# Kernel tuning notes

Hardware: AMD Instinct MI355X
Metric: run time of the kernel (lower is better)

The kernel has to match this reference:

```python
import jax, jax.numpy as jnp
import numpy as np

N = 20000      # num_nodes / scatter_size
F = 128        # dataset_num_features
H = 8          # heads
HID = 64       # hidden_channels
REP = 512      # represent_features
NCLS = 133     # dataset_num_classes
E = 200000     # num edges (== num synapses)
PTS = 4        # points per synapse
P = E * PTS    # total synapse points

# Eval-mode semantics: dropout = identity; PyG MLP BatchNorm with fresh
# running stats (mean=0, var=1, affine=1/0) = identity. GATConv has no
# edge_dim, so edge_attr does not enter the math (kept as an input for parity).

def _glorot(key, shape):
    fan_in, fan_out = shape[0], shape[-1]
    if len(shape) == 3:  # attention vectors [H, C]: PyG treats as (1, H*C)
        fan_in, fan_out = 1, shape[-2] * shape[-1]
    lim = jnp.sqrt(6.0 / (fan_in + fan_out))
    return jax.random.uniform(key, shape, jnp.float32, -lim, lim)


def setup_inputs() -> dict:
    key = jax.random.key(0)
    ks = jax.random.split(key, 20)
    edge_index = jax.random.randint(ks[0], (2, E), 0, N, dtype=jnp.int32)
    edge_attr = jax.random.normal(ks[1], (E, 1), jnp.float32)
    synapse = jax.random.normal(ks[2], (P, 6), jnp.float32)
    # every synapse (edge) owns PTS points -> no empty segments for max-pool
    synapse_index = (jnp.arange(P, dtype=jnp.int32) // PTS)
    inp = {
        "edge_index": edge_index,
        "edge_attr": edge_attr,
        "synapse": synapse,
        "synapse_index": synapse_index,
        "scatter_size": N,
        # learned node embedding (nn.Parameter, xavier)
        "x_param": _glorot(ks[3], (N, F)),
        # GATConv 1: F -> H*HID
        "W1": _glorot(ks[4], (F, H * HID)),
        "att_src1": _glorot(ks[5], (1, H, HID))[0],
        "att_dst1": _glorot(ks[6], (1, H, HID))[0],
        "b1": jnp.zeros((H * HID,), jnp.float32),
        # GATConv 2: H*HID -> REP, heads=1, concat=False
        "W2": _glorot(ks[7], (H * HID, REP)),
        "att_src2": _glorot(ks[8], (1, 1, REP))[0],
        "att_dst2": _glorot(ks[9], (1, 1, REP))[0],
        "b2": jnp.zeros((REP,), jnp.float32),
        # synapse_encoder MLP([6, 256, 512])
        "We1": _glorot(ks[10], (6, 256)),
        "be1": jnp.zeros((256,), jnp.float32),
        "We2": _glorot(ks[11], (256, 512)),
        "be2": jnp.zeros((512,), jnp.float32),
        # classmodel MLP([1536, 512, 133])
        "Wc1": _glorot(ks[12], (1536, 512)),
        "bc1": jnp.zeros((512,), jnp.float32),
        "Wc2": _glorot(ks[13], (512, NCLS)),
        "bc2": jnp.zeros((NCLS,), jnp.float32),
    }
    return inp


def _gat_conv(x, src, dst, n, W, a_src, a_dst, b, heads, ch, concat):
    # x: [n, Fin]; src/dst already include self-loops (PyG default)
    xl = (x @ W).reshape(n, heads, ch)                 # [n, H, C]
    s = jnp.einsum('nhc,hc->nh', xl, a_src)            # alpha_src
    d = jnp.einsum('nhc,hc->nh', xl, a_dst)            # alpha_dst
    alpha = jax.nn.leaky_relu(s[src] + d[dst], negative_slope=0.2)  # [Ee, H]
    amax = jax.ops.segment_max(alpha, dst, num_segments=n)
    ex = jnp.exp(alpha - amax[dst])
    den = jax.ops.segment_sum(ex, dst, num_segments=n)
    a = ex / (den[dst] + 1e-16)                        # segment softmax
    out = jax.ops.segment_sum(xl[src] * a[:, :, None], dst, num_segments=n)
    out = out.reshape(n, heads * ch) if concat else out.mean(axis=1)
    return out + b


def _scatter_mean(vals, idx, n):
    s = jax.ops.segment_sum(vals, idx, num_segments=n)
    cnt = jax.ops.segment_sum(jnp.ones((vals.shape[0],), vals.dtype), idx, num_segments=n)
    return s / jnp.maximum(cnt, 1.0)[:, None]


def reference(edge_index, edge_attr, synapse, synapse_index, scatter_size,
              x_param, W1, att_src1, att_dst1, b1, W2, att_src2, att_dst2, b2,
              We1, be1, We2, be2, Wc1, bc1, Wc2, bc2):
    n = scatter_size
    loop = jnp.arange(n, dtype=edge_index.dtype)
    src = jnp.concatenate([edge_index[0], loop])   # GATConv adds self-loops
    dst = jnp.concatenate([edge_index[1], loop])

    x = jax.nn.elu(_gat_conv(x_param, src, dst, n, W1, att_src1, att_dst1, b1, H, HID, True))
    x = _gat_conv(x, src, dst, n, W2, att_src2, att_dst2, b2, 1, REP, False)   # [n, REP]

    # global_max_pool over synapse points -> one 6-vec per edge
    x_point = jax.ops.segment_max(synapse, synapse_index, num_segments=E)      # [E, 6]
    x_point = jax.nn.relu(x_point @ We1 + be1) @ We2 + be2                      # [E, 512]

    left = _scatter_mean(x_point, edge_index[0], n)
    right = _scatter_mean(x_point, edge_index[1], n)

    final = jnp.concatenate([x, left, right], axis=1)                           # [n, 1536]
    pred = jax.nn.relu(final @ Wc1 + bc1) @ Wc2 + bc2
    return pred
```

## Files before the change

kernel.cpp:

```cpp
#include <hip/hip_runtime.h>
#include <cstddef>

#define NN   20000
#define FEAT 128
#define NH   8
#define NE   200000
#define EE   220000

typedef _Float16 f16;
typedef _Float16 f16x2 __attribute__((ext_vector_type(2)));
typedef _Float16 f16x4 __attribute__((ext_vector_type(4)));
typedef _Float16 f16x8 __attribute__((ext_vector_type(8)));
typedef float    f32x4 __attribute__((ext_vector_type(4)));

__device__ __forceinline__ float lrelu(float a) { return a > 0.f ? a : 0.2f * a; }
__device__ __forceinline__ float rdlane(float v, int l) {
  return __int_as_float(__builtin_amdgcn_readlane(__float_as_int(v), l));
}
__device__ __forceinline__ void gld_lds16(const f16* g, f16* l) {
  __builtin_amdgcn_global_load_lds(
      (const __attribute__((address_space(1))) void*)g,
      (__attribute__((address_space(3))) void*)l, 16, 0, 0);
}

#define QB0 128
#define QB1 (QB0 + 8)
#define QB2 (QB1 + 80)
#define QB3 (QB2 + 64)
#define QB4 (QB3 + 782)
#define QB5 (QB4 + 1250)
__global__ __launch_bounds__(256) void preamble(
    const int* __restrict__ ei, const float* __restrict__ syn,
    const float* __restrict__ W1, const float* __restrict__ xparam,
    const float* __restrict__ W2, const float* __restrict__ We2,
    const float* __restrict__ Wc1, const float* __restrict__ Wc2,
    const float* __restrict__ b2, const float* __restrict__ be2,
    const float* __restrict__ as2, const float* __restrict__ ad2,
    int* __restrict__ dL, int* __restrict__ dR,
    float* __restrict__ xp, f16* __restrict__ W1t, f16* __restrict__ xph,
    f16* __restrict__ WzAt, f16* __restrict__ McatT, f16* __restrict__ Wc2t,
    float* __restrict__ vB, float* __restrict__ vL, float* __restrict__ vR,
    float* __restrict__ ws2, float* __restrict__ wd2)
{
  __shared__ float smem[2112];
  const int b = blockIdx.x, t = threadIdx.x;
  if (b < QB0) {
    float (*As)[68] = (float(*)[68])smem;
    float (*Bs)[64] = (float(*)[64])(smem + 16 * 68);
    const int bb = b;
    const float* A; const float* B; f16* dst; int dstOff, m0, n0;
    if (bb < 64)      { A = W2;  B = Wc1;  dst = WzAt;  dstOff = 0;
                        m0 = (bb >> 3) * 64; n0 = (bb & 7) * 64; }
    else if (bb < 96) { int i = bb - 64; A = We2; B = Wc1 + (size_t)512 * 512;
                        dst = McatT; dstOff = 0;
                        m0 = (i >> 3) * 64; n0 = (i & 7) * 64; }
    else              { int i = bb - 96; A = We2; B = Wc1 + (size_t)1024 * 512;
                        dst = McatT; dstOff = 256;
                        m0 = (i >> 3) * 64; n0 = (i & 7) * 64; }
    const int tx = t & 15, ty = t >> 4;
    float acc[4][4] = {{0.f}};
    float pa[4], pb[4];
#pragma unroll
    for (int i = 0; i < 4; i++) {
      int idx = t + i * 256;
      pa[i] = A[(size_t)(m0 + (idx >> 4)) * 512 + (idx & 15)];
      pb[i] = B[(size_t)(idx >> 6) * 512 + n0 + (idx & 63)];
    }
    for (int k0 = 0; k0 < 512; k0 += 16) {
#pragma unroll
      for (int i = 0; i < 4; i++) {
        int idx = t + i * 256;
        As[idx & 15][idx >> 4] = pa[i];
        Bs[idx >> 6][idx & 63] = pb[i];
      }
      __syncthreads();
      if (k0 + 16 < 512) {
        int kn = k0 + 16;
#pragma unroll
        for (int i = 0; i < 4; i++) {
          int idx = t + i * 256;
          pa[i] = A[(size_t)(m0 + (idx >> 4)) * 512 + kn + (idx & 15)];
          pb[i] = B[(size_t)(kn + (idx >> 6)) * 512 + n0 + (idx & 63)];
        }
      }
#pragma unroll
      for (int kk = 0; kk < 16; kk++) {
        float4 a4 = *(const float4*)&As[kk][ty * 4];
        float4 b4 = *(const float4*)&Bs[kk][tx * 4];
        float av[4] = {a4.x, a4.y, a4.z, a4.w};
        float bv[4] = {b4.x, b4.y, b4.z, b4.w};
#pragma unroll
        for (int i = 0; i < 4; i++)
#pragma unroll
          for (int j = 0; j < 4; j++) acc[i][j] = fmaf(av[i], bv[j], acc[i][j]);
      }
      __syncthreads();
    }
#pragma unroll
    for (int i = 0; i < 4; i++)
#pragma unroll
      for (int j = 0; j < 4; j++)
        dst[(size_t)(n0 + tx * 4 + j) * 512 + dstOff + m0 + ty * 4 + i] = (f16)acc[i][j];
  } else if (b < QB1) {
    int g = (b - QB0) * 256 + t;
    int seg = g >> 9, j = g & 511;
    if (seg == 0) {
      float a = 0.f;
      for (int k = 0; k < 512; k++) a = fmaf(b2[k], Wc1[(size_t)k * 512 + j], a);
      vB[j] = a;
    } else if (seg == 1) {
      float a = 0.f;
      for (int k = 0; k < 512; k++) a = fmaf(be2[k], Wc1[(size_t)(512 + k) * 512 + j], a);
      vL[j] = a;
    } else if (seg == 2) {
      float a = 0.f;
      for (int k = 0; k < 512; k++) a = fmaf(be2[k], Wc1[(size_t)(1024 + k) * 512 + j], a);
      vR[j] = a;
    } else {
      float a = 0.f, c2 = 0.f;
      for (int c = 0; c < 512; c++) {
        float w = W2[(size_t)j * 512 + c];
        a = fmaf(w, as2[c], a);
        c2 = fmaf(w, ad2[c], c2);
      }
      ws2[j] = a; wd2[j] = c2;
    }
  } else if (b < QB2) {
    float (*tile)[33] = (float(*)[33])smem;
    int i0 = b - QB1;
    const int n0 = (i0 % 5) * 32, k0 = (i0 / 5) * 32;
    const int tx = t & 31, ty = t >> 5;
#pragma unroll
    for (int i = 0; i < 4; i++) {
      int k = k0 + ty + i * 8, n = n0 + tx;
      tile[ty + i * 8][tx] = (n < 133) ? Wc2[(size_t)k * 133 + n] : 0.f;
    }
    __syncthreads();
#pragma unroll
    for (int i = 0; i < 4; i++) {
      int n = n0 + ty + i * 8, k = k0 + tx;
      if (n < 133) Wc2t[(size_t)n * 512 + k] = (f16)tile[tx][ty + i * 8];
    }
  } else if (b < QB3) {
    float (*tile)[33] = (float(*)[33])smem;
    int bb = b - QB2;
    const int n0 = (bb & 15) * 32, k0 = (bb >> 4) * 32;
    const int tx = t & 31, ty = t >> 5;
#pragma unroll
    for (int i = 0; i < 4; i++)
      tile[ty + i * 8][tx] = W1[(size_t)(k0 + ty + i * 8) * 512 + n0 + tx];
    __syncthreads();
#pragma unroll
    for (int i = 0; i < 4; i++)
      W1t[(size_t)(n0 + ty + i * 8) * 128 + k0 + tx] = (f16)tile[tx][ty + i * 8];
  } else if (b < QB4) {
    int e = (b - QB3) * 256 + t;
    if (e >= NE) return;
    const float* p = syn + (size_t)e * 24;
    float v[24];
#pragma unroll
    for (int i = 0; i < 6; i++) {
      float4 q = *(const float4*)(p + i * 4);
      v[i*4+0] = q.x; v[i*4+1] = q.y; v[i*4+2] = q.z; v[i*4+3] = q.w;
    }
#pragma unroll
    for (int dd = 0; dd < 6; dd++)
      xp[(size_t)e * 6 + dd] = fmaxf(fmaxf(v[dd], v[6 + dd]), fmaxf(v[12 + dd], v[18 + dd]));
    atomicAdd(&dL[ei[e]], 1);
    atomicAdd(&dR[ei[NE + e]], 1);
  } else {
    int idx = ((b - QB4) * 256 + t) * 8;
    float4 q0 = *(const float4*)(xparam + idx);
    float4 q1 = *(const float4*)(xparam + idx + 4);
    f16x8 o;
    o[0] = (f16)q0.x; o[1] = (f16)q0.y; o[2] = (f16)q0.z; o[3] = (f16)q0.w;
    o[4] = (f16)q1.x; o[5] = (f16)q1.y; o[6] = (f16)q1.z; o[7] = (f16)q1.w;
    *(f16x8*)(xph + idx) = o;
  }
}

__global__ __launch_bounds__(256) void fused1(
    const f16* __restrict__ xph, const f16* __restrict__ W1t, f16* __restrict__ xl1h,
    const float* __restrict__ xp, const float* __restrict__ We1,
    const float* __restrict__ be1,
    const int* __restrict__ oL, const int* __restrict__ eL,
    const int* __restrict__ oR, const int* __restrict__ eR,
    f16* __restrict__ hlrh)
{
  __shared__ __align__(16) f16 smem[7680];
  const int t = threadIdx.x;
  if (blockIdx.x < 1252) {
    f16 (*As)[40] = (f16(*)[40])smem;
    f16 (*Bs)[40] = (f16(*)[40])(smem + 64 * 40);
    const int wave = t >> 6, lane = t & 63;
    const int quad = lane >> 4, mrow = lane & 15;
    const int m0 = (blockIdx.x >> 2) * 64, n0 = (blockIdx.x & 3) * 128;
    f32x4 acc[4][2];
    f32x4 zero4 = {0.f, 0.f, 0.f, 0.f};
#pragma unroll
    for (int i = 0; i < 4; i++)
#pragma unroll
      for (int j = 0; j < 2; j++) acc[i][j] = zero4;
    const int ar = t >> 2, ac = (t & 3) * 8;
    for (int k0 = 0; k0 < FEAT; k0 += 32) {
      {
        int gm = m0 + ar;
        f16x8 v = {0, 0, 0, 0, 0, 0, 0, 0};
        if (gm < NN) v = *(const f16x8*)(xph + (size_t)gm * FEAT + k0 + ac);
        *(f16x8*)&As[ar][ac] = v;
      }
#pragma unroll
      for (int i = 0; i < 2; i++) {
        int idx = t + i * 256;
        int r = idx >> 2, c = (idx & 3) * 8;
        *(f16x8*)&Bs[r][c] = *(const f16x8*)(W1t + (size_t)(n0 + r) * FEAT + k0 + c);
      }
      __syncthreads();
      f16x8 af[4], bf[2];
#pragma unroll
      for (int mt = 0; mt < 4; mt++) af[mt] = *(const f16x8*)&As[mt * 16 + mrow][quad * 8];
#pragma unroll
      for (int nt = 0; nt < 2; nt++) bf[nt] = *(const f16x8*)&Bs[wave * 32 + nt * 16 + mrow][quad * 8];
#pragma unroll
      for (int mt = 0; mt < 4; mt++)
#pragma unroll
        for (int nt = 0; nt < 2; nt++)
          acc[mt][nt] = __builtin_amdgcn_mfma_f32_16x16x32_f16(af[mt], bf[nt], acc[mt][nt], 0, 0, 0);
      __syncthreads();
    }
#pragma unroll
    for (int mt = 0; mt < 4; mt++)
#pragma unroll
      for (int nt = 0; nt < 2; nt++) {
        int col = n0 + wave * 32 + nt * 16 + mrow;
#pragma unroll
        for (int reg = 0; reg < 4; reg++) {
          int row = m0 + mt * 16 + quad * 4 + reg;
          if (row < NN) xl1h[(size_t)row * 512 + col] = (f16)acc[mt][nt][reg];
        }
      }
  } else {
    const int wave = t >> 6, lane = t & 63;
    const int w = (blockIdx.x - 1252) * 4 + wave;
    float4 wv[6];
#pragma unroll
    for (int j = 0; j < 6; j++) wv[j] = *(const float4*)(We1 + j * 256 + 4 * lane);
    const float4 bv = *(const float4*)(be1 + 4 * lane);
#pragma unroll 1
    for (int i = 0; i < 4; i++) {
      const int b = w + i * 10000;
      const int* off; const int* lst; int n;
      if (b < NN) { off = oL; lst = eL; n = b; } else { off = oR; lst = eR; n = b - NN; }
      const int beg = off[n], deg = off[n + 1] - beg;
      float a0 = 0.f, a1 = 0.f, a2 = 0.f, a3 = 0.f;
      for (int base = 0; base < deg; base += 32) {
        const int m = min(32, deg - base);
        float x0 = 0.f, x1 = 0.f, x2 = 0.f, x3 = 0.f, x4 = 0.f, x5 = 0.f;
        if (lane < m) {
          const int e = lst[beg + base + lane];
          const float* pr = xp + (size_t)e * 6;
          float2 p0 = *(const float2*)pr;
          float2 p1 = *(const float2*)(pr + 2);
          float2 p2 = *(const float2*)(pr + 4);
          x0 = p0.x; x1 = p0.y; x2 = p1.x; x3 = p1.y; x4 = p2.x; x5 = p2.y;
        }
        const int ms = __builtin_amdgcn_readfirstlane(m);
        for (int s = 0; s < ms; s++) {
          const float f0 = rdlane(x0, s), f1 = rdlane(x1, s), f2 = rdlane(x2, s);
          const float f3 = rdlane(x3, s), f4 = rdlane(x4, s), f5 = rdlane(x5, s);
          float v0 = bv.x, v1 = bv.y, v2 = bv.z, v3 = bv.w;
          v0 = fmaf(f0, wv[0].x, v0); v1 = fmaf(f0, wv[0].y, v1);
          v2 = fmaf(f0, wv[0].z, v2); v3 = fmaf(f0, wv[0].w, v3);
          v0 = fmaf(f1, wv[1].x, v0); v1 = fmaf(f1, wv[1].y, v1);
          v2 = fmaf(f1, wv[1].z, v2); v3 = fmaf(f1, wv[1].w, v3);
          v0 = fmaf(f2, wv[2].x, v0); v1 = fmaf(f2, wv[2].y, v1);
          v2 = fmaf(f2, wv[2].z, v2); v3 = fmaf(f2, wv[2].w, v3);
          v0 = fmaf(f3, wv[3].x, v0); v1 = fmaf(f3, wv[3].y, v1);
          v2 = fmaf(f3, wv[3].z, v2); v3 = fmaf(f3, wv[3].w, v3);
          v0 = fmaf(f4, wv[4].x, v0); v1 = fmaf(f4, wv[4].y, v1);
          v2 = fmaf(f4, wv[4].z, v2); v3 = fmaf(f4, wv[4].w, v3);
          v0 = fmaf(f5, wv[5].x, v0); v1 = fmaf(f5, wv[5].y, v1);
          v2 = fmaf(f5, wv[5].z, v2); v3 = fmaf(f5, wv[5].w, v3);
          a0 += fmaxf(v0, 0.f); a1 += fmaxf(v1, 0.f);
          a2 += fmaxf(v2, 0.f); a3 += fmaxf(v3, 0.f);
        }
      }
      const float rn = deg > 0 ? 1.f / (float)deg : 0.f;
      f16x4 o;
      o[0] = (f16)(a0 * rn); o[1] = (f16)(a1 * rn);
      o[2] = (f16)(a2 * rn); o[3] = (f16)(a3 * rn);
      *(f16x4*)(hlrh + (size_t)b * 256 + 4 * lane) = o;
    }
  }
}

__global__ __launch_bounds__(256) void fused2(
    const f16* __restrict__ x1h, const f16* __restrict__ WzAt, f16* __restrict__ zh,
    const f16* __restrict__ hlrh, const f16* __restrict__ McatT,
    const int* __restrict__ degL, const int* __restrict__ degR,
    const float* __restrict__ bc1, const float* __restrict__ vB,
    const float* __restrict__ vL, const float* __restrict__ vR, f16* __restrict__ Ph)
{
  __shared__ __align__(16) f16 smem[8192];
  const int t = threadIdx.x;
  const int logical = (blockIdx.x & 7) * 157 + (blockIdx.x >> 3);
  const bool isZ = logical < 628;
  const int bb = isZ ? logical : logical - 628;
  const int wave = t >> 6, lane = t & 63;
  const int wr = wave >> 1, wc = wave & 1;
  const int quad = lane >> 4, mrow = lane & 15;
  const int m0 = (bb >> 2) * 128, n0 = (bb & 3) * 128;
  const f16* Bt = isZ ? WzAt : McatT;
  const int lrow = lane >> 2, lcol = (lane & 3) * 8;
  const int rb0 = wave * 2, rb1 = wave * 2 + 1;
  f16* lA0 = smem + rb0 * 512;
  f16* lA1 = smem + rb1 * 512;
  f16* lB0 = smem + 4096 + rb0 * 512;
  f16* lB1 = smem + 4096 + rb1 * 512;
  const int gar0 = m0 + rb0 * 16 + lrow;
  const int gar1 = m0 + rb1 * 16 + lrow;
  const f16* gB0 = Bt + (size_t)(n0 + rb0 * 16 + lrow) * 512 + lcol;
  const f16* gB1 = Bt + (size_t)(n0 + rb1 * 16 + lrow) * 512 + lcol;

  f32x4 acc[4][4];
  f32x4 zero4 = {0.f, 0.f, 0.f, 0.f};
#pragma unroll
  for (int i = 0; i < 4; i++)
#pragma unroll
    for (int j = 0; j < 4; j++) acc[i][j] = zero4;

#pragma unroll 1
  for (int it = 0; it < 16; ++it) {
    const int k0 = it * 32;
    const f16 *gA0, *gA1;
    if (isZ) {
      gA0 = x1h + (size_t)gar0 * 512 + k0 + lcol;
      gA1 = x1h + (size_t)gar1 * 512 + k0 + lcol;
    } else {
      const int roff = (k0 >> 8) ? NN : 0;
      const int kk = (k0 & 255) + lcol;
      gA0 = hlrh + (size_t)(gar0 + roff) * 256 + kk;
      gA1 = hlrh + (size_t)(gar1 + roff) * 256 + kk;
    }
    gld_lds16(gA0, lA0);
    gld_lds16(gA1, lA1);
    gld_lds16(gB0 + k0, lB0);
    gld_lds16(gB1 + k0, lB1);
    __syncthreads();
    f16x8 af[4], bf[4];
#pragma unroll
    for (int mt = 0; mt < 4; mt++)
      af[mt] = *(const f16x8*)(smem + (wr * 64 + mt * 16 + mrow) * 32 + quad * 8);
#pragma unroll
    for (int nt = 0; nt < 4; nt++)
      bf[nt] = *(const f16x8*)(smem + 4096 + (wc * 64 + nt * 16 + mrow) * 32 + quad * 8);
#pragma unroll
    for (int mt = 0; mt < 4; mt++)
#pragma unroll
      for (int nt = 0; nt < 4; nt++)
        acc[mt][nt] = __builtin_amdgcn_mfma_f32_16x16x32_f16(af[mt], bf[nt], acc[mt][nt], 0, 0, 0);
    __syncthreads();
  }
  if (isZ) {
#pragma unroll
    for (int mt = 0; mt < 4; mt++)
#pragma unroll
      for (int nt = 0; nt < 4; nt++) {
        int col = n0 + wc * 64 + nt * 16 + mrow;
#pragma unroll
        for (int reg = 0; reg < 4; reg++) {
          int row = m0 + wr * 64 + mt * 16 + quad * 4 + reg;
          if (row < NN) zh[(size_t)row * 512 + col] = (f16)acc[mt][nt][reg];
        }
      }
  } else {
#pragma unroll
    for (int mt = 0; mt < 4; mt++)
#pragma unroll
      for (int nt = 0; nt < 4; nt++) {
        int col = n0 + wc * 64 + nt * 16 + mrow;
        float bb2 = bc1[col] + vB[col];
        float vl = vL[col], vr = vR[col];
#pragma unroll
        for (int reg = 0; reg < 4; reg++) {
          int row = m0 + wr * 64 + mt * 16 + quad * 4 + reg;
          if (row >= NN) continue;
          float v = acc[mt][nt][reg] + bb2;
          if (degL[row] > 0) v += vl;
          if (degR[row] > 0) v += vr;
          Ph[(size_t)row * 512 + col] = (f16)v;
        }
      }
  }
}

__global__ __launch_bounds__(256) void mfma_out(
    const f16* __restrict__ A, const f16* __restrict__ Bt,
    const float* __restrict__ bias, float* __restrict__ C, int M)
{
  __shared__ __align__(16) f16 As[64][40];
  __shared__ __align__(16) f16 Bs[128][40];
  const int t = threadIdx.x;
  const int wave = t >> 6, lane = t & 63;
  const int quad = lane >> 4, mrow = lane & 15;
  const int m0 = blockIdx.y * 64, n0 = blockIdx.x * 128;
  f32x4 acc[4][2];
  f32x4 zero4 = {0.f, 0.f, 0.f, 0.f};
#pragma unroll
  for (int i = 0; i < 4; i++)
#pragma unroll
    for (int j = 0; j < 2; j++) acc[i][j] = zero4;
  const int ar = t >> 2, ac = (t & 3) * 8;
  for (int k0 = 0; k0 < 512; k0 += 32) {
    {
      int gm = m0 + ar;
      f16x8 v = {0, 0, 0, 0, 0, 0, 0, 0};
      if (gm < M) v = *(const f16x8*)(A + (size_t)gm * 512 + k0 + ac);
      *(f16x8*)&As[ar][ac] = v;
    }
#pragma unroll
    for (int i = 0; i < 2; i++) {
      int idx = t + i * 256;
      int r = idx >> 2, c = (idx & 3) * 8;
      f16x8 v = {0, 0, 0, 0, 0, 0, 0, 0};
      if (n0 + r < 133) v = *(const f16x8*)(Bt + (size_t)(n0 + r) * 512 + k0 + c);
      *(f16x8*)&Bs[r][c] = v;
    }
    __syncthreads();
    f16x8 af[4], bf[2];
#pragma unroll
    for (int mt = 0; mt < 4; mt++) af[mt] = *(const f16x8*)&As[mt * 16 + mrow][quad * 8];
#pragma unroll
    for (int nt = 0; nt < 2; nt++) bf[nt] = *(const f16x8*)&Bs[wave * 32 + nt * 16 + mrow][quad * 8];
#pragma unroll
    for (int mt = 0; mt < 4; mt++)
#pragma unroll
      for (int nt = 0; nt < 2; nt++)
        acc[mt][nt] = __builtin_amdgcn_mfma_f32_16x16x32_f16(af[mt], bf[nt], acc[mt][nt], 0, 0, 0);
    __syncthreads();
  }
#pragma unroll
  for (int mt = 0; mt < 4; mt++)
#pragma unroll
    for (int nt = 0; nt < 2; nt++) {
      int col = n0 + wave * 32 + nt * 16 + mrow;
      if (col >= 133) continue;
      float bb = bias[col];
#pragma unroll
      for (int reg = 0; reg < 4; reg++) {
        int row = m0 + mt * 16 + quad * 4 + reg;
        if (row < M) C[(size_t)row * 133 + col] = acc[mt][nt][reg] + bb;
      }
    }
}

__global__ __launch_bounds__(1024) void scan_csr(
    const int* __restrict__ dL, const int* __restrict__ dR,
    int* __restrict__ oL, int* __restrict__ oR, int* __restrict__ oA)
{
  const int b = blockIdx.x;
  const int* deg = b == 0 ? dL : dR;
  __shared__ int part[1024];
  const int t = threadIdx.x;
  const int chunk = 20;
  int base = t * chunk;
  int sum = 0;
  for (int i = 0; i < chunk; i++) { int idx = base + i; if (idx < NN) sum += deg[idx]; }
  part[t] = sum;
  __syncthreads();
  for (int o = 1; o < 1024; o <<= 1) {
    int v = (t >= o) ? part[t - o] : 0;
    __syncthreads();
    part[t] += v;
    __syncthreads();
  }
  int run = part[t] - sum;
  if (b == 0) {
    for (int i = 0; i < chunk; i++) {
      int idx = base + i;
      if (idx < NN) { oL[idx] = run; run += deg[idx]; }
    }
    if (t == 0) oL[NN] = part[1023];
  } else {
    for (int i = 0; i < chunk; i++) {
      int idx = base + i;
      if (idx < NN) { oR[idx] = run; oA[idx] = run + idx; run += deg[idx]; }
    }
    if (t == 0) { oR[NN] = part[1023]; oA[NN] = part[1023] + NN; }
  }
}

__global__ __launch_bounds__(256) void fill_csr(
    const int* __restrict__ ei,
    const int* __restrict__ oL, const int* __restrict__ oR, const int* __restrict__ oA,
    int* __restrict__ cL, int* __restrict__ cR,
    int* __restrict__ eL, int* __restrict__ eR, int* __restrict__ snA)
{
  int e = blockIdx.x * 256 + threadIdx.x;
  if (e >= EE) return;
  if (e < NE) {
    int s = ei[e], d = ei[NE + e];
    int p = atomicAdd(&cL[s], 1); eL[oL[s] + p] = e;
    p = atomicAdd(&cR[d], 1);
    eR[oR[d] + p] = e;
    snA[oA[d] + 1 + p] = s;
  } else {
    int n = e - NE;
    snA[oA[n]] = n;
  }
}

__global__ __launch_bounds__(256) void attn_dots1(
    const f16* __restrict__ xlh, const float* __restrict__ asrc,
    const float* __restrict__ adst, float* __restrict__ s, float* __restrict__ d)
{
  int gid = blockIdx.x * 256 + threadIdx.x;
  if (gid >= NN * NH) return;
  int n = gid >> 3, h = gid & 7;
  const f16x2* row = (const f16x2*)(xlh + (size_t)n * 512 + h * 64);
  const float* a1 = asrc + h * 64;
  const float* a2 = adst + h * 64;
  float ss = 0.f, dd = 0.f;
#pragma unroll 8
  for (int j = 0; j < 32; j++) {
    f16x2 p = row[j];
    float v0 = (float)p[0], v1 = (float)p[1];
    ss += v0 * a1[2 * j] + v1 * a1[2 * j + 1];
    dd += v0 * a2[2 * j] + v1 * a2[2 * j + 1];
  }
  s[gid] = ss; d[gid] = dd;
}

__global__ __launch_bounds__(256) void gat_gather1(
    const int* __restrict__ snA, const int* __restrict__ offA,
    const float* __restrict__ s1, const float* __restrict__ d1,
    const f16* __restrict__ xlh, const float* __restrict__ b1,
    const float* __restrict__ ws2, const float* __restrict__ wd2,
    f16* __restrict__ x1h, float* __restrict__ s2, float* __restrict__ d2)
{
  __shared__ int sns[32];
  __shared__ float wls[256];
  __shared__ float red[256], redD[256];
  const int n = blockIdx.x, t = threadIdx.x;
  const int hw = t & 7;
  const int slot = t >> 3;
  const int hf = t >> 5;
  const int beg = offA[n], end = offA[n + 1];
  const int deg = end - beg;
  const float dnw = d1[n * 8 + hw];
  float a0 = 0.f, a1v = 0.f, denp = 0.f;
  for (int base = 0; base < deg; base += 32) {
    int m = min(32, deg - base);
    if (t < 32) sns[t] = (t < m) ? snA[beg + base + t] : 0;
    __syncthreads();
    {
      float w = 0.f;
      if (slot < m) w = __expf(lrelu(s1[sns[slot] * 8 + hw] + dnw));
      wls[t] = w;
      denp += w;
    }
    __syncthreads();
    int m8 = (m + 7) & ~7;
    for (int k = 0; k < m8; k += 8) {
      int ss[8]; float ww[8]; f16x2 pp[8];
#pragma unroll
      for (int u = 0; u < 8; u++) { ss[u] = sns[k + u]; ww[u] = wls[(k + u) * 8 + hf]; }
#pragma unroll
      for (int u = 0; u < 8; u++) pp[u] = *(const f16x2*)(xlh + (size_t)ss[u] * 512 + 2 * t);
#pragma unroll
      for (int u = 0; u < 8; u++) {
        a0  = fmaf(ww[u], (float)pp[u][0], a0);
        a1v = fmaf(ww[u], (float)pp[u][1], a1v);
      }
    }
    __syncthreads();
  }
  red[t] = denp;
  __syncthreads();
  for (int off = 128; off >= 8; off >>= 1) {
    if (t < off) red[t] += red[t + off];
    __syncthreads();
  }
  float rh = 1.f / (red[hf] + 1e-16f);
  __syncthreads();
  float v0 = a0 * rh + b1[2 * t], v1 = a1v * rh + b1[2 * t + 1];
  v0 = v0 > 0.f ? v0 : (__expf(v0) - 1.f);
  v1 = v1 > 0.f ? v1 : (__expf(v1) - 1.f);
  f16x2 o; o[0] = (f16)v0; o[1] = (f16)v1;
  *(f16x2*)(x1h + (size_t)n * 512 + 2 * t) = o;
  red[t]  = v0 * ws2[2 * t] + v1 * ws2[2 * t + 1];
  redD[t] = v0 * wd2[2 * t] + v1 * wd2[2 * t + 1];
  __syncthreads();
  for (int off = 128; off > 0; off >>= 1) {
    if (t < off) { red[t] += red[t + off]; redD[t] += redD[t + off]; }
    __syncthreads();
  }
  if (t == 0) { s2[n] = red[0]; d2[n] = redD[0]; }
}

__global__ __launch_bounds__(256) void gat_gather2(
    const int* __restrict__ snA, const int* __restrict__ offA,
    const float* __restrict__ s2, const float* __restrict__ d2,
    const f16* __restrict__ zh, const f16* __restrict__ Ph,
    f16* __restrict__ h2h)
{
  __shared__ int sns[32];
  __shared__ float wls[32];
  __shared__ float den_sh;
  const int n = blockIdx.x, t = threadIdx.x;
  const int beg = offA[n], end = offA[n + 1];
  const int deg = end - beg;
  const float dn = d2[n];
  float a0 = 0.f, a1v = 0.f, denp = 0.f;
  for (int base = 0; base < deg; base += 32) {
    int m = min(32, deg - base);
    if (t < 32) {
      int sn = (t < m) ? snA[beg + base + t] : 0;
      float w = (t < m) ? __expf(lrelu(s2[sn] + dn)) : 0.f;
      sns[t] = sn;
      wls[t] = w;
      denp += w;
    }
    __syncthreads();
    int m8 = (m + 7) & ~7;
    for (int k = 0; k < m8; k += 8) {
      int ss[8]; float ww[8]; f16x2 pp[8];
#pragma unroll
      for (int u = 0; u < 8; u++) { ss[u] = sns[k + u]; ww[u] = wls[k + u]; }
#pragma unroll
      for (int u = 0; u < 8; u++) pp[u] = *(const f16x2*)(zh + (size_t)ss[u] * 512 + 2 * t);
#pragma unroll
      for (int u = 0; u < 8; u++) {
        a0  = fmaf(ww[u], (float)pp[u][0], a0);
        a1v = fmaf(ww[u], (float)pp[u][1], a1v);
      }
    }
    __syncthreads();
  }
  if (t < 64) {
    denp += __shfl_xor(denp, 16);
    denp += __shfl_xor(denp, 8);
    denp += __shfl_xor(denp, 4);
    denp += __shfl_xor(denp, 2);
    denp += __shfl_xor(denp, 1);
    if (t == 0) den_sh = denp;
  }
  __syncthreads();
  float rn = 1.f / (den_sh + 1e-16f);
  f16x2 pv = *(const f16x2*)(Ph + (size_t)n * 512 + 2 * t);
  float v0 = fmaxf(a0  * rn + (float)pv[0], 0.f);
  float v1 = fmaxf(a1v * rn + (float)pv[1], 0.f);
  f16x2 o; o[0] = (f16)v0; o[1] = (f16)v1;
  *(f16x2*)(h2h + (size_t)n * 512 + 2 * t) = o;
}

extern "C" void kernel_launch(void* const* d_in, const int* in_sizes, int n_in,
                              void* d_out, int out_size, void* d_ws, size_t ws_size,
                              hipStream_t stream) {
  const int*   edge_index = (const int*)d_in[0];
  const float* synapse    = (const float*)d_in[2];
  const float* x_param = (const float*)d_in[5];
  const float* W1      = (const float*)d_in[6];
  const float* as1     = (const float*)d_in[7];
  const float* ad1     = (const float*)d_in[8];
  const float* b1      = (const float*)d_in[9];
  const float* W2      = (const float*)d_in[10];
  const float* as2     = (const float*)d_in[11];
  const float* ad2     = (const float*)d_in[12];
  const float* b2      = (const float*)d_in[13];
  const float* We1     = (const float*)d_in[14];
  const float* be1     = (const float*)d_in[15];
  const float* We2     = (const float*)d_in[16];
  const float* be2     = (const float*)d_in[17];
  const float* Wc1     = (const float*)d_in[18];
  const float* bc1     = (const float*)d_in[19];
  const float* Wc2     = (const float*)d_in[20];
  const float* bc2     = (const float*)d_in[21];
  float* out_p = (float*)d_out;

  char* p = (char*)d_ws;
  float* xp    = (float*)p; p += (size_t)NE * 6 * 4;
  float* s1    = (float*)p; p += (size_t)NN * 8 * 4;
  float* d1    = (float*)p; p += (size_t)NN * 8 * 4;
  float* s2    = (float*)p; p += (size_t)NN * 4;
  float* d2    = (float*)p; p += (size_t)NN * 4;
  float* vB    = (float*)p; p += 512 * 4;
  float* vL    = (float*)p; p += 512 * 4;
  float* vR    = (float*)p; p += 512 * 4;
  float* ws2   = (float*)p; p += 512 * 4;
  float* wd2   = (float*)p; p += 512 * 4;
  f16* xph     = (f16*)p; p += (size_t)NN * FEAT * 2;
  f16* xl1h    = (f16*)p; p += (size_t)NN * 512 * 2;
  f16* x1h     = (f16*)p; p += (size_t)NN * 512 * 2;
  f16* zh      = (f16*)p; p += (size_t)NN * 512 * 2;
  f16* h2h     = (f16*)p; p += (size_t)NN * 512 * 2;
  f16* Phb     = (f16*)p; p += (size_t)NN * 512 * 2;
  f16* hlrh    = (f16*)p; p += (size_t)2 * NN * 256 * 2;
  f16* W1t     = (f16*)p; p += (size_t)512 * FEAT * 2;
  f16* WzAt    = (f16*)p; p += (size_t)512 * 512 * 2;
  f16* McatT   = (f16*)p; p += (size_t)512 * 512 * 2;
  f16* Wc2t    = (f16*)p; p += (size_t)133 * 512 * 2;
  int* degL    = (int*)p;
  int* degR    = degL + NN;
  int* curL    = degR + NN;
  int* curR    = curL + NN;
  int* offL    = curR + NN;
  int* offR    = offL + NN + 1;
  int* offA    = offR + NN + 1;
  int* edgeL   = offA + NN + 1;
  int* edgeR   = edgeL + NE;
  int* snA     = edgeR + NE;

  hipMemsetAsync(degL, 0, (size_t)4 * NN * sizeof(int), stream);

  preamble<<<QB5, 256, 0, stream>>>(
      edge_index, synapse, W1, x_param, W2, We2, Wc1, Wc2, b2, be2, as2, ad2,
      degL, degR, xp, W1t, xph, WzAt, McatT, Wc2t, vB, vL, vR, ws2, wd2);
  scan_csr<<<2, 1024, 0, stream>>>(degL, degR, offL, offR, offA);
  fill_csr<<<(EE + 255) / 256, 256, 0, stream>>>(edge_index, offL, offR, offA,
                                                 curL, curR, edgeL, edgeR, snA);
  fused1<<<1252 + 2500, 256, 0, stream>>>(xph, W1t, xl1h, xp, We1, be1,
                                          offL, edgeL, offR, edgeR, hlrh);
  attn_dots1<<<(NN * NH + 255) / 256, 256, 0, stream>>>(xl1h, as1, ad1, s1, d1);
  gat_gather1<<<NN, 256, 0, stream>>>(snA, offA, s1, d1, xl1h, b1, ws2, wd2,
                                      x1h, s2, d2);
  fused2<<<1256, 256, 0, stream>>>(x1h, WzAt, zh, hlrh, McatT,
                                   degL, degR, bc1, vB, vL, vR, Phb);
  gat_gather2<<<NN, 256, 0, stream>>>(snA, offA, s2, d2, zh, Phb, h2h);
  mfma_out<<<dim3(2, 313), 256, 0, stream>>>(h2h, Wc2t, bc2, out_p, NN);
}
```

Baseline: 431.3 us.

## Process one node per wavefront in GAT gather kernels with 16-byte row loads

Both GAT aggregation kernels move from one 256-thread block per node to one 64-lane wavefront per node, four nodes per block. Each lane now loads 8 halves at once. Neighbor indices are broadcast with readlane instead of going through shared memory, and all block barriers and LDS reductions are replaced by wave shuffles. Attention weights are recomputed per lane instead of being shared through LDS. This is meant to cut sync overhead and small-load inefficiency at the cost of redundant exp work and longer serial loops per wave.

```diff
diff --git a/kernel.cpp b/kernel.cpp
--- a/kernel.cpp
+++ b/kernel.cpp
@@ -538,64 +538,73 @@
     const float* __restrict__ ws2, const float* __restrict__ wd2,
     f16* __restrict__ x1h, float* __restrict__ s2, float* __restrict__ d2)
 {
-  __shared__ int sns[32];
-  __shared__ float wls[256];
-  __shared__ float red[256], redD[256];
-  const int n = blockIdx.x, t = threadIdx.x;
-  const int hw = t & 7;
-  const int slot = t >> 3;
-  const int hf = t >> 5;
-  const int beg = offA[n], end = offA[n + 1];
-  const int deg = end - beg;
-  const float dnw = d1[n * 8 + hw];
-  float a0 = 0.f, a1v = 0.f, denp = 0.f;
-  for (int base = 0; base < deg; base += 32) {
-    int m = min(32, deg - base);
-    if (t < 32) sns[t] = (t < m) ? snA[beg + base + t] : 0;
-    __syncthreads();
-    {
-      float w = 0.f;
-      if (slot < m) w = __expf(lrelu(s1[sns[slot] * 8 + hw] + dnw));
-      wls[t] = w;
-      denp += w;
-    }
-    __syncthreads();
-    int m8 = (m + 7) & ~7;
-    for (int k = 0; k < m8; k += 8) {
-      int ss[8]; float ww[8]; f16x2 pp[8];
-#pragma unroll
-      for (int u = 0; u < 8; u++) { ss[u] = sns[k + u]; ww[u] = wls[(k + u) * 8 + hf]; }
-#pragma unroll
-      for (int u = 0; u < 8; u++) pp[u] = *(const f16x2*)(xlh + (size_t)ss[u] * 512 + 2 * t);
-#pragma unroll
-      for (int u = 0; u < 8; u++) {
-        a0  = fmaf(ww[u], (float)pp[u][0], a0);
-        a1v = fmaf(ww[u], (float)pp[u][1], a1v);
-      }
-    }
-    __syncthreads();
-  }
-  red[t] = denp;
-  __syncthreads();
-  for (int off = 128; off >= 8; off >>= 1) {
-    if (t < off) red[t] += red[t + off];
-    __syncthreads();
-  }
-  float rh = 1.f / (red[hf] + 1e-16f);
-  __syncthreads();
-  float v0 = a0 * rh + b1[2 * t], v1 = a1v * rh + b1[2 * t + 1];
-  v0 = v0 > 0.f ? v0 : (__expf(v0) - 1.f);
-  v1 = v1 > 0.f ? v1 : (__expf(v1) - 1.f);
-  f16x2 o; o[0] = (f16)v0; o[1] = (f16)v1;
-  *(f16x2*)(x1h + (size_t)n * 512 + 2 * t) = o;
-  red[t]  = v0 * ws2[2 * t] + v1 * ws2[2 * t + 1];
-  redD[t] = v0 * wd2[2 * t] + v1 * wd2[2 * t + 1];
-  __syncthreads();
-  for (int off = 128; off > 0; off >>= 1) {
-    if (t < off) { red[t] += red[t + off]; redD[t] += redD[t + off]; }
-    __syncthreads();
-  }
-  if (t == 0) { s2[n] = red[0]; d2[n] = redD[0]; }
+  const int t = threadIdx.x;
+  const int wave = t >> 6, lane = t & 63;
+  const int n = blockIdx.x * 4 + wave;
+  const int hf = lane >> 3;
+  const float dnw = d1[n * 8 + hf];
+  const int beg = offA[n], deg = offA[n + 1] - beg;
+  float acc[8] = {0.f};
+  float den = 0.f;
+  for (int base = 0; base < deg; base += 64) {
+    const int m = min(64, deg - base);
+    int me = 0;
+    if (lane < m) me = snA[beg + base + lane];
+    const int ms = __builtin_amdgcn_readfirstlane(m);
+    int s = 0;
+    for (; s + 4 <= ms; s += 4) {
+      int sn[4]; float sv[4]; f16x8 row[4];
+#pragma unroll
+      for (int u = 0; u < 4; u++) sn[u] = __builtin_amdgcn_readlane(me, s + u);
+#pragma unroll
+      for (int u = 0; u < 4; u++) sv[u] = s1[sn[u] * 8 + hf];
+#pragma unroll
+      for (int u = 0; u < 4; u++) row[u] = *(const f16x8*)(xlh + (size_t)sn[u] * 512 + lane * 8);
+#pragma unroll
+      for (int u = 0; u < 4; u++) {
+        float w = __expf(lrelu(sv[u] + dnw));
+        den += w;
+#pragma unroll
+        for (int j = 0; j < 8; j++) acc[j] = fmaf(w, (float)row[u][j], acc[j]);
+      }
+    }
+    for (; s < ms; ++s) {
+      int sn = __builtin_amdgcn_readlane(me, s);
+      float sv = s1[sn * 8 + hf];
+      f16x8 row = *(const f16x8*)(xlh + (size_t)sn * 512 + lane * 8);
+      float w = __expf(lrelu(sv + dnw));
+      den += w;
+#pragma unroll
+      for (int j = 0; j < 8; j++) acc[j] = fmaf(w, (float)row[j], acc[j]);
+    }
+  }
+  const float rh = 1.f / (den + 1e-16f);
+  float4 bv0 = *(const float4*)(b1 + lane * 8);
+  float4 bv1 = *(const float4*)(b1 + lane * 8 + 4);
+  float bb[8] = {bv0.x, bv0.y, bv0.z, bv0.w, bv1.x, bv1.y, bv1.z, bv1.w};
+  float4 wsa = *(const float4*)(ws2 + lane * 8);
+  float4 wsb = *(const float4*)(ws2 + lane * 8 + 4);
+  float4 wda = *(const float4*)(wd2 + lane * 8);
+  float4 wdb = *(const float4*)(wd2 + lane * 8 + 4);
+  float wsv[8] = {wsa.x, wsa.y, wsa.z, wsa.w, wsb.x, wsb.y, wsb.z, wsb.w};
+  float wdv[8] = {wda.x, wda.y, wda.z, wda.w, wdb.x, wdb.y, wdb.z, wdb.w};
+  f16x8 o;
+  float ps = 0.f, pd = 0.f;
+#pragma unroll
+  for (int j = 0; j < 8; j++) {
+    float v = acc[j] * rh + bb[j];
+    v = v > 0.f ? v : (__expf(v) - 1.f);
+    o[j] = (f16)v;
+    ps = fmaf(v, wsv[j], ps);
+    pd = fmaf(v, wdv[j], pd);
+  }
+  *(f16x8*)(x1h + (size_t)n * 512 + lane * 8) = o;
+#pragma unroll
+  for (int off = 32; off > 0; off >>= 1) {
+    ps += __shfl_xor(ps, off);
+    pd += __shfl_xor(pd, off);
+  }
+  if (lane == 0) { s2[n] = ps; d2[n] = pd; }
 }
 
 __global__ __launch_bounds__(256) void gat_gather2(
@@ -604,54 +613,54 @@
     const f16* __restrict__ zh, const f16* __restrict__ Ph,
     f16* __restrict__ h2h)
 {
-  __shared__ int sns[32];
-  __shared__ float wls[32];
-  __shared__ float den_sh;
-  const int n = blockIdx.x, t = threadIdx.x;
-  const int beg = offA[n], end = offA[n + 1];
-  const int deg = end - beg;
+  const int t = threadIdx.x;
+  const int wave = t >> 6, lane = t & 63;
+  const int n = blockIdx.x * 4 + wave;
   const float dn = d2[n];
-  float a0 = 0.f, a1v = 0.f, denp = 0.f;
-  for (int base = 0; base < deg; base += 32) {
-    int m = min(32, deg - base);
-    if (t < 32) {
-      int sn = (t < m) ? snA[beg + base + t] : 0;
-      float w = (t < m) ? __expf(lrelu(s2[sn] + dn)) : 0.f;
-      sns[t] = sn;
-      wls[t] = w;
-      denp += w;
-    }
-    __syncthreads();
-    int m8 = (m + 7) & ~7;
-    for (int k = 0; k < m8; k += 8) {
-      int ss[8]; float ww[8]; f16x2 pp[8];
-#pragma unroll
-      for (int u = 0; u < 8; u++) { ss[u] = sns[k + u]; ww[u] = wls[k + u]; }
-#pragma unroll
-      for (int u = 0; u < 8; u++) pp[u] = *(const f16x2*)(zh + (size_t)ss[u] * 512 + 2 * t);
-#pragma unroll
-      for (int u = 0; u < 8; u++) {
-        a0  = fmaf(ww[u], (float)pp[u][0], a0);
-        a1v = fmaf(ww[u], (float)pp[u][1], a1v);
-      }
-    }
-    __syncthreads();
-  }
-  if (t < 64) {
-    denp += __shfl_xor(denp, 16);
-    denp += __shfl_xor(denp, 8);
-    denp += __shfl_xor(denp, 4);
-    denp += __shfl_xor(denp, 2);
-    denp += __shfl_xor(denp, 1);
-    if (t == 0) den_sh = denp;
-  }
-  __syncthreads();
-  float rn = 1.f / (den_sh + 1e-16f);
-  f16x2 pv = *(const f16x2*)(Ph + (size_t)n * 512 + 2 * t);
-  float v0 = fmaxf(a0  * rn + (float)pv[0], 0.f);
-  float v1 = fmaxf(a1v * rn + (float)pv[1], 0.f);
-  f16x2 o; o[0] = (f16)v0; o[1] = (f16)v1;
-  *(f16x2*)(h2h + (size_t)n * 512 + 2 * t) = o;
+  const int beg = offA[n], deg = offA[n + 1] - beg;
+  float acc[8] = {0.f};
+  float den = 0.f;
+  for (int base = 0; base < deg; base += 64) {
+    const int m = min(64, deg - base);
+    int me = 0;
+    if (lane < m) me = snA[beg + base + lane];
+    const int ms = __builtin_amdgcn_readfirstlane(m);
+    int s = 0;
+    for (; s + 4 <= ms; s += 4) {
+      int sn[4]; float sv[4]; f16x8 row[4];
+#pragma unroll
+      for (int u = 0; u < 4; u++) sn[u] = __builtin_amdgcn_readlane(me, s + u);
+#pragma unroll
+      for (int u = 0; u < 4; u++) sv[u] = s2[sn[u]];
+#pragma unroll
+      for (int u = 0; u < 4; u++) row[u] = *(const f16x8*)(zh + (size_t)sn[u] * 512 + lane * 8);
+#pragma unroll
+      for (int u = 0; u < 4; u++) {
+        float w = __expf(lrelu(sv[u] + dn));
+        den += w;
+#pragma unroll
+        for (int j = 0; j < 8; j++) acc[j] = fmaf(w, (float)row[u][j], acc[j]);
+      }
+    }
+    for (; s < ms; ++s) {
+      int sn = __builtin_amdgcn_readlane(me, s);
+      float sv = s2[sn];
+      f16x8 row = *(const f16x8*)(zh + (size_t)sn * 512 + lane * 8);
+      float w = __expf(lrelu(sv + dn));
+      den += w;
+#pragma unroll
+      for (int j = 0; j < 8; j++) acc[j] = fmaf(w, (float)row[j], acc[j]);
+    }
+  }
+  const float rn = 1.f / (den + 1e-16f);
+  f16x8 pv = *(const f16x8*)(Ph + (size_t)n * 512 + lane * 8);
+  f16x8 o;
+#pragma unroll
+  for (int j = 0; j < 8; j++) {
+    float v = fmaxf(acc[j] * rn + (float)pv[j], 0.f);
+    o[j] = (f16)v;
+  }
+  *(f16x8*)(h2h + (size_t)n * 512 + lane * 8) = o;
 }
 
 extern "C" void kernel_launch(void* const* d_in, const int* in_sizes, int n_in,
@@ -722,10 +731,10 @@
   fused1<<<1252 + 2500, 256, 0, stream>>>(xph, W1t, xl1h, xp, We1, be1,
                                           offL, edgeL, offR, edgeR, hlrh);
   attn_dots1<<<(NN * NH + 255) / 256, 256, 0, stream>>>(xl1h, as1, ad1, s1, d1);
-  gat_gather1<<<NN, 256, 0, stream>>>(snA, offA, s1, d1, xl1h, b1, ws2, wd2,
-                                      x1h, s2, d2);
+  gat_gather1<<<5000, 256, 0, stream>>>(snA, offA, s1, d1, xl1h, b1, ws2, wd2,
+                                        x1h, s2, d2);
   fused2<<<1256, 256, 0, stream>>>(x1h, WzAt, zh, hlrh, McatT,
                                    degL, degR, bc1, vB, vL, vR, Phb);
-  gat_gather2<<<NN, 256, 0, stream>>>(snA, offA, s2, d2, zh, Phb, h2h);
+  gat_gather2<<<5000, 256, 0, stream>>>(snA, offA, s2, d2, zh, Phb, h2h);
   mfma_out<<<dim3(2, 313), 256, 0, stream>>>(h2h, Wc2t, bc2, out_p, NN);
 }
```

Result: faster. 418.4 us (-3.0%).
